# Optimization experiments

Hardware: AMD Instinct MI355X
Metric: run time of the kernel (lower is better)

## Reference

```python
import jax, jax.numpy as jnp
import numpy as np

V = 32          # num_variables
T = 48          # num_time_bins
D = 512         # d_model
H = 8           # num_heads
HD = D // H     # head_dim = 64
OD = 16         # observation_dim
B = 4


def setup_inputs() -> dict:
    key = jax.random.key(0)
    ks = jax.random.split(key, 20)
    s = 0.02
    inp = {
        'h': jax.random.normal(ks[0], (B, T, V, D), jnp.float32),
        'observation_state': jax.random.normal(ks[1], (B, T, V, 2), jnp.float32),
        'Wq': jax.random.normal(ks[2], (D, D), jnp.float32) * s,
        'bq': jnp.zeros((D,), jnp.float32),
        'Wk': jax.random.normal(ks[3], (D, D), jnp.float32) * s,
        'bk': jnp.zeros((D,), jnp.float32),
        'Wv': jax.random.normal(ks[4], (D, D), jnp.float32) * s,
        'bv': jnp.zeros((D,), jnp.float32),
        'Wo': jax.random.normal(ks[5], (D, D), jnp.float32) * s,
        'bo': jnp.zeros((D,), jnp.float32),
        'Woq': jax.random.normal(ks[6], (2, H * OD), jnp.float32) * 0.5,
        'boq': jnp.zeros((H * OD,), jnp.float32),
        'Wok': jax.random.normal(ks[7], (2, H * OD), jnp.float32) * 0.5,
        'bok': jnp.zeros((H * OD,), jnp.float32),
        'variable_bias': jax.random.normal(ks[8], (H, V, V), jnp.float32) * 0.01,
        'relative_time_bias': jax.random.normal(ks[9], (H, 2 * T - 1), jnp.float32) * 0.01,
    }
    return inp


def reference(h, observation_state, Wq, bq, Wk, bk, Wv, bv, Wo, bo,
              Woq, boq, Wok, bok, variable_bias, relative_time_bias):
    N = T * V
    scale = 1.0 / np.sqrt(HD)
    obs_scale = 1.0 / np.sqrt(OD)

    # static index buffers (constants)
    flat_var_ids = jnp.tile(jnp.arange(V), T)                       # [N]
    flat_time_ids = jnp.repeat(jnp.arange(T), V)                    # [N]
    rel_index = flat_time_ids[:, None] - flat_time_ids[None, :] + (T - 1)  # [N,N]

    fh = h.reshape(B, N, D)
    fo = observation_state.reshape(B, N, 2)

    def heads(x, nh, hd):
        return x.reshape(B, N, nh, hd).transpose(0, 2, 1, 3)  # [B,H,N,hd]

    q = heads(fh @ Wq + bq, H, HD)
    k = heads(fh @ Wk + bk, H, HD)
    v = heads(fh @ Wv + bv, H, HD)
    oq = heads(fo @ Woq + boq, H, OD)
    ok = heads(fo @ Wok + bok, H, OD)

    content = jnp.einsum('bhnd,bhmd->bhnm', q, k) * scale
    obs = jnp.einsum('bhnd,bhmd->bhnm', oq, ok) * obs_scale
    var_scores = variable_bias[:, flat_var_ids[:, None], flat_var_ids[None, :]]  # [H,N,N]
    time_scores = relative_time_bias[:, rel_index]                                # [H,N,N]

    scores = content + obs + var_scores[None] + time_scores[None]
    attn = jax.nn.softmax(scores, axis=-1)  # dropout off (inference)
    out = jnp.einsum('bhnm,bhmd->bhnd', attn, v)
    out = out.transpose(0, 2, 1, 3).reshape(B, N, D)
    out = out @ Wo + bo
    return out.reshape(B, T, V, D)
```

## Files before the change

### kernel.cpp

```cpp
#include <hip/hip_runtime.h>
#include <math.h>

typedef __bf16 bf16x8 __attribute__((ext_vector_type(8)));
typedef float f32x4 __attribute__((ext_vector_type(4)));

#define NB 4
#define NT 48
#define NV 32
#define ND 512
#define NH 8
#define NN 1536
#define NBN 6144
#define KQ 96

#define GLOAD_LDS(g, l) \
    __builtin_amdgcn_global_load_lds( \
        (const __attribute__((address_space(1))) void*)(g), \
        (__attribute__((address_space(3))) void*)(l), 16, 0, 0)

__global__ __launch_bounds__(256) void conv_h(const float* __restrict__ h,
                                              __bf16* __restrict__ o)
{
    int t = blockIdx.x * 256 + threadIdx.x;
    const float4* src = (const float4*)h + (size_t)t * 2;
    float4 a = src[0], b = src[1];
    __bf16 r[8] = {(__bf16)a.x, (__bf16)a.y, (__bf16)a.z, (__bf16)a.w,
                   (__bf16)b.x, (__bf16)b.y, (__bf16)b.z, (__bf16)b.w};
    *(uint4*)(o + (size_t)t * 8) = *(uint4*)r;
}

__global__ __launch_bounds__(256) void conv_w(
    const float* __restrict__ Wq, const float* __restrict__ Wk,
    const float* __restrict__ Wv, const float* __restrict__ Wo,
    const float* __restrict__ bq, const float* __restrict__ bk,
    const float* __restrict__ bv,
    __bf16* __restrict__ WcatT, __bf16* __restrict__ WoT,
    float* __restrict__ biascat)
{
    __shared__ float ts[64][68];
    const int tid = threadIdx.x;
    const int bx = blockIdx.x;
    const int p = bx >> 6, tile = bx & 63;
    const int k0 = (tile >> 3) * 64, c0 = (tile & 7) * 64;
    const float* W = (p == 0) ? Wq : (p == 1) ? Wk : (p == 2) ? Wv : Wo;
    #pragma unroll
    for (int i = 0; i < 4; i++) {
        int r = (tid >> 4) + i * 16;
        float4 v = *(const float4*)(W + (size_t)(k0 + r) * 512 + c0 + (tid & 15) * 4);
        *(float4*)&ts[r][(tid & 15) * 4] = v;
    }
    __syncthreads();
    __bf16 tmp[16];
    #pragma unroll
    for (int j = 0; j < 16; j++)
        tmp[j] = (__bf16)ts[(tid & 3) * 16 + j][tid >> 2];
    int crow = c0 + (tid >> 2);
    __bf16* dst = (p < 3)
        ? WcatT + ((size_t)(p * 512 + crow)) * 512 + k0 + (tid & 3) * 16
        : WoT   + ((size_t)crow) * 512 + k0 + (tid & 3) * 16;
    *(uint4*)dst = *(uint4*)tmp;
    *(uint4*)(dst + 8) = *(uint4*)(tmp + 8);
    if (p < 3 && k0 == 0 && tid < 64) {
        const float* bb = (p == 0) ? bq : (p == 1) ? bk : bv;
        biascat[p * 512 + c0 + tid] = bb[c0 + tid];
    }
}

__global__ __launch_bounds__(256) void oqok_pad(
    const float* __restrict__ obs,
    const float* __restrict__ Woq, const float* __restrict__ boq,
    const float* __restrict__ Wok, const float* __restrict__ bok,
    __bf16* __restrict__ qo, __bf16* __restrict__ ko)
{
    int t = blockIdx.x * 256 + threadIdx.x;
    int j = t & 31, hh = (t >> 5) & 7, bn = t >> 8;
    int b = bn / NN, n = bn % NN;
    size_t base = (((size_t)b * NH + hh) * NN + n) * KQ + 64 + j;
    if (j < 16) {
        float o0 = obs[bn * 2], o1 = obs[bn * 2 + 1];
        int f = hh * 16 + j;
        float oqv = o0 * Woq[f] + o1 * Woq[128 + f] + boq[f];
        float okv = o0 * Wok[f] + o1 * Wok[128 + f] + bok[f];
        qo[base] = (__bf16)(0.25f * oqv);
        ko[base] = (__bf16)okv;
    } else {
        qo[base] = (__bf16)0.0f;
        ko[base] = (__bf16)0.0f;
    }
}

template<int TM>
__global__ __launch_bounds__(256) void gemm_mfma(
    const __bf16* __restrict__ A, const __bf16* __restrict__ Bt,
    const float* __restrict__ bias, float* __restrict__ Cout,
    __bf16* __restrict__ qo, __bf16* __restrict__ ko, __bf16* __restrict__ vo,
    int mode)
{
    constexpr int MT = TM / 32;
    __shared__ __bf16 As[TM][32];
    __shared__ __bf16 Bs[128][32];
    const int tid = threadIdx.x;
    const int w = tid >> 6, lane = tid & 63;
    const int quad = lane >> 4, l16 = lane & 15;
    const int wm = w >> 1, wn = w & 1;
    const int n0 = blockIdx.x * 128, m0 = blockIdx.y * TM;

    const int sm = tid >> 2;
    const int sk = ((tid & 3) ^ ((sm >> 1) & 3)) * 8;
    const __bf16* aptr = A  + (size_t)(m0 + sm) * 512 + sk;
    const __bf16* bptr = Bt + (size_t)(n0 + sm) * 512 + sk;
    __bf16* lA = (__bf16*)As + tid * 8;
    __bf16* lB = (__bf16*)Bs + tid * 8;

    f32x4 zero4 = {0.f, 0.f, 0.f, 0.f};
    f32x4 acc[MT][4];
    #pragma unroll
    for (int i = 0; i < MT; i++)
        #pragma unroll
        for (int j = 0; j < 4; j++) acc[i][j] = zero4;

    for (int kt = 0; kt < 512; kt += 32) {
        __syncthreads();
        GLOAD_LDS(aptr + kt, lA);
        if (TM == 128) GLOAD_LDS(aptr + 64 * 512 + kt, lA + 2048);
        GLOAD_LDS(bptr + kt, lB);
        GLOAD_LDS(bptr + 64 * 512 + kt, lB + 2048);
        __syncthreads();
        bf16x8 af[MT], bfr[4];
        #pragma unroll
        for (int mt = 0; mt < MT; mt++) {
            int rr = wm * (TM / 2) + mt * 16 + l16;
            af[mt] = *(const bf16x8*)&As[rr][(quad ^ ((rr >> 1) & 3)) * 8];
        }
        #pragma unroll
        for (int nt = 0; nt < 4; nt++) {
            int rr = wn * 64 + nt * 16 + l16;
            bfr[nt] = *(const bf16x8*)&Bs[rr][(quad ^ ((rr >> 1) & 3)) * 8];
        }
        #pragma unroll
        for (int mt = 0; mt < MT; mt++)
            #pragma unroll
            for (int nt = 0; nt < 4; nt++)
                acc[mt][nt] = __builtin_amdgcn_mfma_f32_16x16x32_bf16(
                    af[mt], bfr[nt], acc[mt][nt], 0, 0, 0);
    }

    #pragma unroll
    for (int mt = 0; mt < MT; mt++) {
        #pragma unroll
        for (int nt = 0; nt < 4; nt++) {
            int c = n0 + wn * 64 + nt * 16 + l16;
            float bia = bias[c];
            #pragma unroll
            for (int r = 0; r < 4; r++) {
                int row = m0 + wm * (TM / 2) + mt * 16 + quad * 4 + r;
                float val = acc[mt][nt][r] + bia;
                if (mode == 0) {
                    Cout[(size_t)row * 512 + c] = val;
                } else {
                    int p = c >> 9, f = c & 511, hh = f >> 6, d = f & 63;
                    int b = row / NN, nn = row % NN;
                    size_t bhn = ((size_t)b * NH + hh) * NN + nn;
                    if (p == 0)      qo[bhn * KQ + d] = (__bf16)(val * 0.125f);
                    else if (p == 1) ko[bhn * KQ + d] = (__bf16)val;
                    else             vo[bhn * 64 + d] = (__bf16)val;
                }
            }
        }
    }
}

__global__ __launch_bounds__(256, 4) void attn_mfma(
    const __bf16* __restrict__ qp, const __bf16* __restrict__ kp,
    const __bf16* __restrict__ vp, const float* __restrict__ varb,
    const float* __restrict__ rtb, __bf16* __restrict__ aout)
{
    __shared__ __bf16 Ks[64][104];
    __shared__ __bf16 Vt[64][72];
    __shared__ __bf16 Ps[64][72];
    __shared__ float  rts[96];

    const int tid = threadIdx.x;
    const int w = tid >> 6, lane = tid & 63;
    const int quad = lane >> 4, l16 = lane & 15;
    const int qt = blockIdx.x, bh = blockIdx.y;
    const int b = bh >> 3, h = bh & 7;
    const int n0 = qt * 64;

    const __bf16* qb = qp + ((size_t)bh * NN + n0) * KQ;
    const __bf16* kb = kp + (size_t)bh * NN * KQ;
    const __bf16* vb = vp + (size_t)bh * NN * 64;

    if (tid < 95) rts[tid] = rtb[h * 95 + tid];

    bf16x8 aq[3];
    #pragma unroll
    for (int ks = 0; ks < 3; ks++)
        aq[ks] = *(const bf16x8*)(qb + (size_t)(w * 16 + l16) * KQ + ks * 32 + quad * 8);

    float vb0[4], vb1[4];
    #pragma unroll
    for (int r = 0; r < 4; r++) {
        int rm = (w * 16 + quad * 4 + r) & 31;
        vb0[r] = varb[h * 1024 + rm * 32 + l16];
        vb1[r] = varb[h * 1024 + rm * 32 + 16 + l16];
    }
    const int tn = 2 * qt + (w >> 1);

    f32x4 zero4 = {0.f, 0.f, 0.f, 0.f};
    f32x4 o[4];
    float lpart[4];
    #pragma unroll
    for (int i = 0; i < 4; i++) { o[i] = zero4; lpart[i] = 0.f; }

    const int kr0 = tid / 12,         kc0 = (tid % 12) * 8;
    const int kr1 = (tid + 256) / 12, kc1 = ((tid + 256) % 12) * 8;
    const int kr2 = (tid + 512) / 12, kc2 = ((tid + 512) % 12) * 8;
    const int vp2 = tid & 31, vd8 = tid >> 5;

    uint4 kreg[3], vreg[2];
    kreg[0] = *(const uint4*)(kb + (size_t)kr0 * KQ + kc0);
    kreg[1] = *(const uint4*)(kb + (size_t)kr1 * KQ + kc1);
    kreg[2] = *(const uint4*)(kb + (size_t)kr2 * KQ + kc2);
    vreg[0] = *(const uint4*)(vb + (size_t)(2 * vp2) * 64 + vd8 * 8);
    vreg[1] = *(const uint4*)(vb + (size_t)(2 * vp2 + 1) * 64 + vd8 * 8);
    {
        *(uint4*)&Ks[kr0][kc0] = kreg[0];
        *(uint4*)&Ks[kr1][kc1] = kreg[1];
        *(uint4*)&Ks[kr2][kc2] = kreg[2];
        const unsigned short* lo = (const unsigned short*)&vreg[0];
        const unsigned short* hi = (const unsigned short*)&vreg[1];
        #pragma unroll
        for (int j = 0; j < 8; j++) {
            unsigned int pk = (unsigned int)lo[j] | ((unsigned int)hi[j] << 16);
            *(unsigned int*)&Vt[vd8 * 8 + j][2 * vp2] = pk;
        }
    }
    __syncthreads();

    for (int mt = 0; mt < 24; mt++) {
        if (mt < 23) {
            const __bf16* kbn = kb + (size_t)(mt + 1) * 64 * KQ;
            const __bf16* vbn = vb + (size_t)(mt + 1) * 64 * 64;
            kreg[0] = *(const uint4*)(kbn + (size_t)kr0 * KQ + kc0);
            kreg[1] = *(const uint4*)(kbn + (size_t)kr1 * KQ + kc1);
            kreg[2] = *(const uint4*)(kbn + (size_t)kr2 * KQ + kc2);
            vreg[0] = *(const uint4*)(vbn + (size_t)(2 * vp2) * 64 + vd8 * 8);
            vreg[1] = *(const uint4*)(vbn + (size_t)(2 * vp2 + 1) * 64 + vd8 * 8);
        }
        f32x4 sc[4];
        #pragma unroll
        for (int ct = 0; ct < 4; ct++) {
            f32x4 d = zero4;
            #pragma unroll
            for (int ks = 0; ks < 3; ks++) {
                bf16x8 bf = *(const bf16x8*)&Ks[ct * 16 + l16][ks * 32 + quad * 8];
                d = __builtin_amdgcn_mfma_f32_16x16x32_bf16(aq[ks], bf, d, 0, 0, 0);
            }
            sc[ct] = d;
        }
        float tb0 = rts[tn - 2 * mt + 47];
        float tb1 = rts[tn - 2 * mt + 46];
        #pragma unroll
        for (int ct = 0; ct < 4; ct++) {
            float tb = (ct & 2) ? tb1 : tb0;
            #pragma unroll
            for (int r = 0; r < 4; r++) {
                float s = sc[ct][r] + tb + ((ct & 1) ? vb1[r] : vb0[r]);
                float p = __expf(s);
                lpart[r] += p;
                Ps[w * 16 + quad * 4 + r][ct * 16 + l16] = (__bf16)p;
            }
        }
        #pragma unroll
        for (int ks = 0; ks < 2; ks++) {
            bf16x8 pf = *(const bf16x8*)&Ps[w * 16 + l16][ks * 32 + quad * 8];
            #pragma unroll
            for (int dt = 0; dt < 4; dt++) {
                bf16x8 vf = *(const bf16x8*)&Vt[dt * 16 + l16][ks * 32 + quad * 8];
                o[dt] = __builtin_amdgcn_mfma_f32_16x16x32_bf16(pf, vf, o[dt], 0, 0, 0);
            }
        }
        __syncthreads();
        if (mt < 23) {
            *(uint4*)&Ks[kr0][kc0] = kreg[0];
            *(uint4*)&Ks[kr1][kc1] = kreg[1];
            *(uint4*)&Ks[kr2][kc2] = kreg[2];
            const unsigned short* lo = (const unsigned short*)&vreg[0];
            const unsigned short* hi = (const unsigned short*)&vreg[1];
            #pragma unroll
            for (int j = 0; j < 8; j++) {
                unsigned int pk = (unsigned int)lo[j] | ((unsigned int)hi[j] << 16);
                *(unsigned int*)&Vt[vd8 * 8 + j][2 * vp2] = pk;
            }
        }
        __syncthreads();
    }

    #pragma unroll
    for (int r = 0; r < 4; r++) {
        float l = lpart[r];
        l += __shfl_xor(l, 1);
        l += __shfl_xor(l, 2);
        l += __shfl_xor(l, 4);
        l += __shfl_xor(l, 8);
        float inv = 1.0f / l;
        int n = n0 + w * 16 + quad * 4 + r;
        size_t base = ((size_t)b * NN + n) * 512 + h * 64 + l16;
        #pragma unroll
        for (int dt = 0; dt < 4; dt++)
            aout[base + dt * 16] = (__bf16)(o[dt][r] * inv);
    }
}

extern "C" void kernel_launch(void* const* d_in, const int* in_sizes, int n_in,
                              void* d_out, int out_size, void* d_ws, size_t ws_size,
                              hipStream_t stream)
{
    const float* h_   = (const float*)d_in[0];
    const float* obs  = (const float*)d_in[1];
    const float* Wq   = (const float*)d_in[2];
    const float* bq   = (const float*)d_in[3];
    const float* Wk   = (const float*)d_in[4];
    const float* bk   = (const float*)d_in[5];
    const float* Wv   = (const float*)d_in[6];
    const float* bv   = (const float*)d_in[7];
    const float* Wo   = (const float*)d_in[8];
    const float* bo   = (const float*)d_in[9];
    const float* Woq  = (const float*)d_in[10];
    const float* boq  = (const float*)d_in[11];
    const float* Wok  = (const float*)d_in[12];
    const float* bok  = (const float*)d_in[13];
    const float* varb = (const float*)d_in[14];
    const float* rtb  = (const float*)d_in[15];
    float* out = (float*)d_out;

    char* ws = (char*)d_ws;
    __bf16* qo      = (__bf16*)ws;                 ws += (size_t)32 * NN * KQ * 2;
    __bf16* ko      = (__bf16*)ws;                 ws += (size_t)32 * NN * KQ * 2;
    __bf16* vo      = (__bf16*)ws;                 ws += (size_t)32 * NN * 64 * 2;
    __bf16* h_bf    = (__bf16*)ws;                 ws += (size_t)NBN * 512 * 2;
    __bf16* attnout = (__bf16*)ws;                 ws += (size_t)NBN * 512 * 2;
    __bf16* WcatT   = (__bf16*)ws;                 ws += (size_t)1536 * 512 * 2;
    __bf16* WoT     = (__bf16*)ws;                 ws += (size_t)512 * 512 * 2;
    float*  biascat = (float*)ws;                  ws += 1536 * 4;

    conv_h<<<dim3(1536), dim3(256), 0, stream>>>(h_, h_bf);
    conv_w<<<dim3(256), dim3(256), 0, stream>>>(Wq, Wk, Wv, Wo, bq, bk, bv,
                                                WcatT, WoT, biascat);
    gemm_mfma<128><<<dim3(12, 48), dim3(256), 0, stream>>>(
        h_bf, WcatT, biascat, nullptr, qo, ko, vo, 1);
    oqok_pad<<<dim3(6144), dim3(256), 0, stream>>>(obs, Woq, boq, Wok, bok, qo, ko);
    attn_mfma<<<dim3(24, 32), dim3(256), 0, stream>>>(qo, ko, vo, varb, rtb, attnout);
    gemm_mfma<64><<<dim3(4, 96), dim3(256), 0, stream>>>(
        attnout, WoT, bo, out, nullptr, nullptr, nullptr, 0);
}
```

Baseline: 215.2 us.

## Restructure QKV layout and stream K/V tiles to LDS via direct loads

The QKV GEMM now writes a plain row-major bf16 buffer, with the query scale folded into the converted weights. Separate kernels then build a padded K buffer that carries the observation-key features, and a transposed V buffer. The attention kernel computes the observation-query part in registers and fills K/V tiles with global_load_lds into XOR-swizzled LDS in place of register staging, and it drops the occupancy hint in launch bounds. This is meant to cut scattered GEMM epilogue stores and LDS bank conflicts, at the cost of an extra launch, losing the register prefetch overlap, and leaving two barriers per tile.

```diff
diff --git a/kernel.cpp b/kernel.cpp
--- a/kernel.cpp
+++ b/kernel.cpp
@@ -11,7 +11,6 @@
 #define NH 8
 #define NN 1536
 #define NBN 6144
-#define KQ 96
 
 #define GLOAD_LDS(g, l) \
     __builtin_amdgcn_global_load_lds( \
@@ -43,6 +42,7 @@
     const int p = bx >> 6, tile = bx & 63;
     const int k0 = (tile >> 3) * 64, c0 = (tile & 7) * 64;
     const float* W = (p == 0) ? Wq : (p == 1) ? Wk : (p == 2) ? Wv : Wo;
+    const float scale = (p == 0) ? 0.125f : 1.0f;
     #pragma unroll
     for (int i = 0; i < 4; i++) {
         int r = (tid >> 4) + i * 16;
@@ -53,7 +53,7 @@
     __bf16 tmp[16];
     #pragma unroll
     for (int j = 0; j < 16; j++)
-        tmp[j] = (__bf16)ts[(tid & 3) * 16 + j][tid >> 2];
+        tmp[j] = (__bf16)(ts[(tid & 3) * 16 + j][tid >> 2] * scale);
     int crow = c0 + (tid >> 2);
     __bf16* dst = (p < 3)
         ? WcatT + ((size_t)(p * 512 + crow)) * 512 + k0 + (tid & 3) * 16
@@ -62,43 +62,74 @@
     *(uint4*)(dst + 8) = *(uint4*)(tmp + 8);
     if (p < 3 && k0 == 0 && tid < 64) {
         const float* bb = (p == 0) ? bq : (p == 1) ? bk : bv;
-        biascat[p * 512 + c0 + tid] = bb[c0 + tid];
-    }
-}
-
-__global__ __launch_bounds__(256) void oqok_pad(
-    const float* __restrict__ obs,
-    const float* __restrict__ Woq, const float* __restrict__ boq,
+        biascat[p * 512 + c0 + tid] = bb[c0 + tid] * scale;
+    }
+}
+
+__global__ __launch_bounds__(256) void kprep(
+    const __bf16* __restrict__ qkv, const float* __restrict__ obs,
     const float* __restrict__ Wok, const float* __restrict__ bok,
-    __bf16* __restrict__ qo, __bf16* __restrict__ ko)
+    __bf16* __restrict__ kx)
 {
     int t = blockIdx.x * 256 + threadIdx.x;
-    int j = t & 31, hh = (t >> 5) & 7, bn = t >> 8;
-    int b = bn / NN, n = bn % NN;
-    size_t base = (((size_t)b * NH + hh) * NN + n) * KQ + 64 + j;
-    if (j < 16) {
-        float o0 = obs[bn * 2], o1 = obs[bn * 2 + 1];
-        int f = hh * 16 + j;
-        float oqv = o0 * Woq[f] + o1 * Woq[128 + f] + boq[f];
-        float okv = o0 * Wok[f] + o1 * Wok[128 + f] + bok[f];
-        qo[base] = (__bf16)(0.25f * oqv);
-        ko[base] = (__bf16)okv;
+    int row = t / 6, seg = t - row * 6;
+    int b = row / 12288, rem = row - b * 12288;
+    int h = rem >> 11 ? 0 : 0;
+    h = rem / 1536;
+    int n = rem - h * 1536;
+    __bf16* dst = kx + (size_t)row * 96 + seg * 16;
+    if (seg < 4) {
+        const __bf16* src = qkv + ((size_t)(b * NN + n)) * 1536 + 512 + h * 64 + seg * 16;
+        *(uint4*)dst       = *(const uint4*)src;
+        *(uint4*)(dst + 8) = *(const uint4*)(src + 8);
+    } else if (seg == 4) {
+        float o0 = obs[(size_t)(b * NN + n) * 2];
+        float o1 = obs[(size_t)(b * NN + n) * 2 + 1];
+        int f = h * 16;
+        __bf16 tmp[16];
+        #pragma unroll
+        for (int j = 0; j < 16; j++)
+            tmp[j] = (__bf16)(o0 * Wok[f + j] + o1 * Wok[128 + f + j] + bok[f + j]);
+        *(uint4*)dst       = *(uint4*)tmp;
+        *(uint4*)(dst + 8) = *(uint4*)(tmp + 8);
     } else {
-        qo[base] = (__bf16)0.0f;
-        ko[base] = (__bf16)0.0f;
-    }
-}
-
-template<int TM>
+        uint4 z = {0, 0, 0, 0};
+        *(uint4*)dst       = z;
+        *(uint4*)(dst + 8) = z;
+    }
+}
+
+__global__ __launch_bounds__(256) void vtrans(const __bf16* __restrict__ qkv,
+                                              __bf16* __restrict__ vt)
+{
+    __shared__ __bf16 ts[64][72];
+    const int tid = threadIdx.x;
+    const int nt = blockIdx.x, bh = blockIdx.y;
+    const int b = bh >> 3, h = bh & 7;
+    const int n0 = nt * 64;
+    const __bf16* src = qkv + ((size_t)(b * NN + n0 + (tid >> 2))) * 1536
+                            + 1024 + h * 64 + (tid & 3) * 16;
+    *(uint4*)&ts[tid >> 2][(tid & 3) * 16]     = *(const uint4*)src;
+    *(uint4*)&ts[tid >> 2][(tid & 3) * 16 + 8] = *(const uint4*)(src + 8);
+    __syncthreads();
+    __bf16 tmp[16];
+    #pragma unroll
+    for (int j = 0; j < 16; j++)
+        tmp[j] = ts[(tid & 3) * 16 + j][tid >> 2];
+    __bf16* dst = vt + ((size_t)bh * 64 + (tid >> 2)) * 1536 + n0 + (tid & 3) * 16;
+    *(uint4*)dst       = *(uint4*)tmp;
+    *(uint4*)(dst + 8) = *(uint4*)(tmp + 8);
+}
+
+template<int TM, bool BF16OUT>
 __global__ __launch_bounds__(256) void gemm_mfma(
     const __bf16* __restrict__ A, const __bf16* __restrict__ Bt,
-    const float* __restrict__ bias, float* __restrict__ Cout,
-    __bf16* __restrict__ qo, __bf16* __restrict__ ko, __bf16* __restrict__ vo,
-    int mode)
+    const float* __restrict__ bias, float* __restrict__ Cf,
+    __bf16* __restrict__ Cbf, int Ncol)
 {
     constexpr int MT = TM / 32;
-    __shared__ __bf16 As[TM][32];
-    __shared__ __bf16 Bs[128][32];
+    __shared__ __align__(16) __bf16 As[TM][32];
+    __shared__ __align__(16) __bf16 Bs[128][32];
     const int tid = threadIdx.x;
     const int w = tid >> 6, lane = tid & 63;
     const int quad = lane >> 4, l16 = lane & 15;
@@ -155,30 +186,24 @@
             for (int r = 0; r < 4; r++) {
                 int row = m0 + wm * (TM / 2) + mt * 16 + quad * 4 + r;
                 float val = acc[mt][nt][r] + bia;
-                if (mode == 0) {
-                    Cout[(size_t)row * 512 + c] = val;
-                } else {
-                    int p = c >> 9, f = c & 511, hh = f >> 6, d = f & 63;
-                    int b = row / NN, nn = row % NN;
-                    size_t bhn = ((size_t)b * NH + hh) * NN + nn;
-                    if (p == 0)      qo[bhn * KQ + d] = (__bf16)(val * 0.125f);
-                    else if (p == 1) ko[bhn * KQ + d] = (__bf16)val;
-                    else             vo[bhn * 64 + d] = (__bf16)val;
-                }
+                if (BF16OUT) Cbf[(size_t)row * Ncol + c] = (__bf16)val;
+                else         Cf[(size_t)row * Ncol + c] = val;
             }
         }
     }
 }
 
-__global__ __launch_bounds__(256, 4) void attn_mfma(
-    const __bf16* __restrict__ qp, const __bf16* __restrict__ kp,
-    const __bf16* __restrict__ vp, const float* __restrict__ varb,
-    const float* __restrict__ rtb, __bf16* __restrict__ aout)
-{
-    __shared__ __bf16 Ks[64][104];
-    __shared__ __bf16 Vt[64][72];
-    __shared__ __bf16 Ps[64][72];
-    __shared__ float  rts[96];
+__global__ __launch_bounds__(256) void attn_mfma(
+    const __bf16* __restrict__ qkv, const __bf16* __restrict__ kx,
+    const __bf16* __restrict__ vt, const float* __restrict__ obs,
+    const float* __restrict__ Woq, const float* __restrict__ boq,
+    const float* __restrict__ varb, const float* __restrict__ rtb,
+    __bf16* __restrict__ aout)
+{
+    __shared__ __align__(16) __bf16 Ks[64][128];
+    __shared__ __align__(16) __bf16 Vs[64][64];
+    __shared__ __align__(16) __bf16 Ps[64][64];
+    __shared__ float rts[96];
 
     const int tid = threadIdx.x;
     const int w = tid >> 6, lane = tid & 63;
@@ -187,16 +212,36 @@
     const int b = bh >> 3, h = bh & 7;
     const int n0 = qt * 64;
 
-    const __bf16* qb = qp + ((size_t)bh * NN + n0) * KQ;
-    const __bf16* kb = kp + (size_t)bh * NN * KQ;
-    const __bf16* vb = vp + (size_t)bh * NN * 64;
-
     if (tid < 95) rts[tid] = rtb[h * 95 + tid];
 
+    const size_t qrow = (size_t)(b * NN + n0 + w * 16 + l16);
     bf16x8 aq[3];
-    #pragma unroll
-    for (int ks = 0; ks < 3; ks++)
-        aq[ks] = *(const bf16x8*)(qb + (size_t)(w * 16 + l16) * KQ + ks * 32 + quad * 8);
+    aq[0] = *(const bf16x8*)(qkv + qrow * 1536 + h * 64 + quad * 8);
+    aq[1] = *(const bf16x8*)(qkv + qrow * 1536 + h * 64 + 32 + quad * 8);
+    {
+        uint4 a2u = {0u, 0u, 0u, 0u};
+        if (quad < 2) {
+            float o0 = obs[qrow * 2], o1 = obs[qrow * 2 + 1];
+            int f = h * 16 + quad * 8;
+            float4 w0a = *(const float4*)(Woq + f);
+            float4 w0b = *(const float4*)(Woq + f + 4);
+            float4 w1a = *(const float4*)(Woq + 128 + f);
+            float4 w1b = *(const float4*)(Woq + 128 + f + 4);
+            float4 ba  = *(const float4*)(boq + f);
+            float4 bb2 = *(const float4*)(boq + f + 4);
+            __bf16 tmp[8];
+            tmp[0] = (__bf16)(0.25f * (o0 * w0a.x + o1 * w1a.x + ba.x));
+            tmp[1] = (__bf16)(0.25f * (o0 * w0a.y + o1 * w1a.y + ba.y));
+            tmp[2] = (__bf16)(0.25f * (o0 * w0a.z + o1 * w1a.z + ba.z));
+            tmp[3] = (__bf16)(0.25f * (o0 * w0a.w + o1 * w1a.w + ba.w));
+            tmp[4] = (__bf16)(0.25f * (o0 * w0b.x + o1 * w1b.x + bb2.x));
+            tmp[5] = (__bf16)(0.25f * (o0 * w0b.y + o1 * w1b.y + bb2.y));
+            tmp[6] = (__bf16)(0.25f * (o0 * w0b.z + o1 * w1b.z + bb2.z));
+            tmp[7] = (__bf16)(0.25f * (o0 * w0b.w + o1 * w1b.w + bb2.w));
+            a2u = *(uint4*)tmp;
+        }
+        aq[2] = *(bf16x8*)&a2u;
+    }
 
     float vb0[4], vb1[4];
     #pragma unroll
@@ -207,54 +252,44 @@
     }
     const int tn = 2 * qt + (w >> 1);
 
+    const int ck = (tid & 15) ^ ((tid >> 4) & 7);
+    const __bf16* kbase = kx + (size_t)bh * NN * 96 + ck * 8;
+    const int cv = (tid & 7) ^ ((tid >> 3) & 7);
+    const __bf16* vbase = vt + (size_t)bh * 64 * 1536 + cv * 8;
+
     f32x4 zero4 = {0.f, 0.f, 0.f, 0.f};
     f32x4 o[4];
     float lpart[4];
     #pragma unroll
     for (int i = 0; i < 4; i++) { o[i] = zero4; lpart[i] = 0.f; }
 
-    const int kr0 = tid / 12,         kc0 = (tid % 12) * 8;
-    const int kr1 = (tid + 256) / 12, kc1 = ((tid + 256) % 12) * 8;
-    const int kr2 = (tid + 512) / 12, kc2 = ((tid + 512) % 12) * 8;
-    const int vp2 = tid & 31, vd8 = tid >> 5;
-
-    uint4 kreg[3], vreg[2];
-    kreg[0] = *(const uint4*)(kb + (size_t)kr0 * KQ + kc0);
-    kreg[1] = *(const uint4*)(kb + (size_t)kr1 * KQ + kc1);
-    kreg[2] = *(const uint4*)(kb + (size_t)kr2 * KQ + kc2);
-    vreg[0] = *(const uint4*)(vb + (size_t)(2 * vp2) * 64 + vd8 * 8);
-    vreg[1] = *(const uint4*)(vb + (size_t)(2 * vp2 + 1) * 64 + vd8 * 8);
-    {
-        *(uint4*)&Ks[kr0][kc0] = kreg[0];
-        *(uint4*)&Ks[kr1][kc1] = kreg[1];
-        *(uint4*)&Ks[kr2][kc2] = kreg[2];
-        const unsigned short* lo = (const unsigned short*)&vreg[0];
-        const unsigned short* hi = (const unsigned short*)&vreg[1];
-        #pragma unroll
-        for (int j = 0; j < 8; j++) {
-            unsigned int pk = (unsigned int)lo[j] | ((unsigned int)hi[j] << 16);
-            *(unsigned int*)&Vt[vd8 * 8 + j][2 * vp2] = pk;
-        }
-    }
-    __syncthreads();
+    char* ldsK = (char*)Ks;
+    char* ldsV = (char*)Vs;
 
     for (int mt = 0; mt < 24; mt++) {
-        if (mt < 23) {
-            const __bf16* kbn = kb + (size_t)(mt + 1) * 64 * KQ;
-            const __bf16* vbn = vb + (size_t)(mt + 1) * 64 * 64;
-            kreg[0] = *(const uint4*)(kbn + (size_t)kr0 * KQ + kc0);
-            kreg[1] = *(const uint4*)(kbn + (size_t)kr1 * KQ + kc1);
-            kreg[2] = *(const uint4*)(kbn + (size_t)kr2 * KQ + kc2);
-            vreg[0] = *(const uint4*)(vbn + (size_t)(2 * vp2) * 64 + vd8 * 8);
-            vreg[1] = *(const uint4*)(vbn + (size_t)(2 * vp2 + 1) * 64 + vd8 * 8);
-        }
+        const int m0 = mt * 64;
+        __syncthreads();
+        #pragma unroll
+        for (int i = 0; i < 4; i++) {
+            int row = i * 16 + (tid >> 4);
+            GLOAD_LDS(kbase + (size_t)(m0 + row) * 96, ldsK + i * 4096 + tid * 16);
+        }
+        #pragma unroll
+        for (int i = 0; i < 2; i++) {
+            int row = i * 32 + (tid >> 3);
+            GLOAD_LDS(vbase + (size_t)row * 1536 + m0, ldsV + i * 4096 + tid * 16);
+        }
+        __syncthreads();
+
         f32x4 sc[4];
         #pragma unroll
         for (int ct = 0; ct < 4; ct++) {
             f32x4 d = zero4;
+            int row = ct * 16 + l16;
             #pragma unroll
             for (int ks = 0; ks < 3; ks++) {
-                bf16x8 bf = *(const bf16x8*)&Ks[ct * 16 + l16][ks * 32 + quad * 8];
+                bf16x8 bf = *(const bf16x8*)((const char*)Ks + row * 256
+                                + (((ks * 4 + quad) ^ (row & 7)) * 16));
                 d = __builtin_amdgcn_mfma_f32_16x16x32_bf16(aq[ks], bf, d, 0, 0, 0);
             }
             sc[ct] = d;
@@ -269,32 +304,23 @@
                 float s = sc[ct][r] + tb + ((ct & 1) ? vb1[r] : vb0[r]);
                 float p = __expf(s);
                 lpart[r] += p;
-                Ps[w * 16 + quad * 4 + r][ct * 16 + l16] = (__bf16)p;
+                int rowp = w * 16 + quad * 4 + r;
+                int pc = ((ct * 2) + (l16 >> 3)) ^ (rowp & 7);
+                Ps[rowp][pc * 8 + (l16 & 7)] = (__bf16)p;
             }
         }
         #pragma unroll
         for (int ks = 0; ks < 2; ks++) {
-            bf16x8 pf = *(const bf16x8*)&Ps[w * 16 + l16][ks * 32 + quad * 8];
+            int rowr = w * 16 + l16;
+            bf16x8 pf = *(const bf16x8*)&Ps[rowr][((ks * 4 + quad) ^ (l16 & 7)) * 8];
             #pragma unroll
             for (int dt = 0; dt < 4; dt++) {
-                bf16x8 vf = *(const bf16x8*)&Vt[dt * 16 + l16][ks * 32 + quad * 8];
+                int rw = dt * 16 + l16;
+                bf16x8 vf = *(const bf16x8*)((const char*)Vs + rw * 128
+                                + (((ks * 4 + quad) ^ (rw & 7)) * 16));
                 o[dt] = __builtin_amdgcn_mfma_f32_16x16x32_bf16(pf, vf, o[dt], 0, 0, 0);
             }
         }
-        __syncthreads();
-        if (mt < 23) {
-            *(uint4*)&Ks[kr0][kc0] = kreg[0];
-            *(uint4*)&Ks[kr1][kc1] = kreg[1];
-            *(uint4*)&Ks[kr2][kc2] = kreg[2];
-            const unsigned short* lo = (const unsigned short*)&vreg[0];
-            const unsigned short* hi = (const unsigned short*)&vreg[1];
-            #pragma unroll
-            for (int j = 0; j < 8; j++) {
-                unsigned int pk = (unsigned int)lo[j] | ((unsigned int)hi[j] << 16);
-                *(unsigned int*)&Vt[vd8 * 8 + j][2 * vp2] = pk;
-            }
-        }
-        __syncthreads();
     }
 
     #pragma unroll
@@ -336,22 +362,24 @@
     float* out = (float*)d_out;
 
     char* ws = (char*)d_ws;
-    __bf16* qo      = (__bf16*)ws;                 ws += (size_t)32 * NN * KQ * 2;
-    __bf16* ko      = (__bf16*)ws;                 ws += (size_t)32 * NN * KQ * 2;
-    __bf16* vo      = (__bf16*)ws;                 ws += (size_t)32 * NN * 64 * 2;
     __bf16* h_bf    = (__bf16*)ws;                 ws += (size_t)NBN * 512 * 2;
+    __bf16* qkv     = (__bf16*)ws;                 ws += (size_t)NBN * 1536 * 2;
+    __bf16* kx      = (__bf16*)ws;                 ws += ((size_t)32 * NN * 96 + 64) * 2;
     __bf16* attnout = (__bf16*)ws;                 ws += (size_t)NBN * 512 * 2;
     __bf16* WcatT   = (__bf16*)ws;                 ws += (size_t)1536 * 512 * 2;
     __bf16* WoT     = (__bf16*)ws;                 ws += (size_t)512 * 512 * 2;
     float*  biascat = (float*)ws;                  ws += 1536 * 4;
+    __bf16* vt      = h_bf;
 
     conv_h<<<dim3(1536), dim3(256), 0, stream>>>(h_, h_bf);
     conv_w<<<dim3(256), dim3(256), 0, stream>>>(Wq, Wk, Wv, Wo, bq, bk, bv,
                                                 WcatT, WoT, biascat);
-    gemm_mfma<128><<<dim3(12, 48), dim3(256), 0, stream>>>(
-        h_bf, WcatT, biascat, nullptr, qo, ko, vo, 1);
-    oqok_pad<<<dim3(6144), dim3(256), 0, stream>>>(obs, Woq, boq, Wok, bok, qo, ko);
-    attn_mfma<<<dim3(24, 32), dim3(256), 0, stream>>>(qo, ko, vo, varb, rtb, attnout);
-    gemm_mfma<64><<<dim3(4, 96), dim3(256), 0, stream>>>(
-        attnout, WoT, bo, out, nullptr, nullptr, nullptr, 0);
-}
+    gemm_mfma<128, true><<<dim3(12, 48), dim3(256), 0, stream>>>(
+        h_bf, WcatT, biascat, nullptr, qkv, 1536);
+    kprep<<<dim3(1152), dim3(256), 0, stream>>>(qkv, obs, Wok, bok, kx);
+    vtrans<<<dim3(24, 32), dim3(256), 0, stream>>>(qkv, vt);
+    attn_mfma<<<dim3(24, 32), dim3(256), 0, stream>>>(qkv, kx, vt, obs, Woq, boq,
+                                                      varb, rtb, attnout);
+    gemm_mfma<64, false><<<dim3(4, 96), dim3(256), 0, stream>>>(
+        attnout, WoT, bo, out, nullptr, 512);
+}
```

Measured after the change: 187.8 us. 1.15x faster.
